# Kernel optimization log

Hardware: AMD Instinct MI355X
Metric: run time of the kernel (lower is better)

Reference implementation:

```python
import jax, jax.numpy as jnp
import numpy as np

B, S, D, H = 4, 2048, 1024, 16
DH = D // H
MAX_SEQ = 2048
OUT = 1024


def setup_inputs() -> dict:
    key = jax.random.key(0)
    ks = jax.random.split(key, 10)
    inp = {
        "x": jax.random.normal(ks[0], (B, S, D), dtype=jnp.float32),
        "src_key_padding_mask": jnp.ones((B, S), dtype=jnp.float32),  # 1 = valid token
        "pos_emb": jax.random.normal(ks[1], (1, MAX_SEQ, D), dtype=jnp.float32),
        "ln_gamma": jnp.ones((D,), dtype=jnp.float32),
        "ln_beta": jnp.zeros((D,), dtype=jnp.float32),
        "in_proj_weight": jax.random.normal(ks[2], (3 * D, D), dtype=jnp.float32) * (1.0 / np.sqrt(D)),
        "in_proj_bias": jnp.zeros((3 * D,), dtype=jnp.float32),
        "out_proj_weight": jax.random.normal(ks[3], (D, D), dtype=jnp.float32) * (1.0 / np.sqrt(D)),
        "out_proj_bias": jnp.zeros((D,), dtype=jnp.float32),
        "to_out_weight": jax.random.normal(ks[4], (OUT, D), dtype=jnp.float32) * (1.0 / np.sqrt(D)),
        "to_out_bias": jnp.zeros((OUT,), dtype=jnp.float32),
    }
    return inp


def _layernorm(x, gamma, beta, eps=1e-5):
    mu = jnp.mean(x, axis=-1, keepdims=True)
    var = jnp.mean(jnp.square(x - mu), axis=-1, keepdims=True)
    return (x - mu) * jax.lax.rsqrt(var + eps) * gamma + beta


def reference(x, src_key_padding_mask, pos_emb, ln_gamma, ln_beta,
              in_proj_weight, in_proj_bias, out_proj_weight, out_proj_bias,
              to_out_weight, to_out_bias):
    seq = x.shape[1]
    xn = _layernorm(x, ln_gamma, ln_beta)
    xp = xn + pos_emb[:, :seq, :]  # [B,S,D]

    # PyTorch quirk: 1.0 - mask.long() is a FLOAT tensor -> treated as ADDITIVE mask.
    add_mask = (1.0 - src_key_padding_mask)[:, None, None, :]  # [B,1,1,S]

    qkv = xp @ in_proj_weight.T + in_proj_bias  # [B,S,3D]
    q, k, v = jnp.split(qkv, 3, axis=-1)
    # [B,H,S,DH]
    q = q.reshape(B, seq, H, DH).transpose(0, 2, 1, 3)
    k = k.reshape(B, seq, H, DH).transpose(0, 2, 1, 3)
    v = v.reshape(B, seq, H, DH).transpose(0, 2, 1, 3)

    scores = jnp.einsum("bhqd,bhkd->bhqk", q, k) / jnp.sqrt(jnp.float32(DH))
    scores = scores + add_mask
    attn = jax.nn.softmax(scores, axis=-1)
    o = jnp.einsum("bhqk,bhkd->bhqd", attn, v)  # [B,H,S,DH]
    o = o.transpose(0, 2, 1, 3).reshape(B, seq, D)
    attn_out = o @ out_proj_weight.T + out_proj_bias

    return (xp + attn_out) @ to_out_weight.T + to_out_bias
```

## Files before the change

kernel.cpp:

```cpp
#include <hip/hip_runtime.h>
#include <stdint.h>
#include <stddef.h>

typedef unsigned short u16;
typedef __bf16 bf16x8 __attribute__((ext_vector_type(8)));
typedef float floatx4 __attribute__((ext_vector_type(4)));

#define B_  4
#define S_  2048
#define D_  1024
#define H_  16
#define DH_ 64

__device__ __forceinline__ float b2f(u16 u) {
  union { unsigned u; float f; } c; c.u = ((unsigned)u) << 16; return c.f;
}
__device__ __forceinline__ u16 f2b(float f) {
  union { float f; unsigned u; } c; c.f = f;
  unsigned u = c.u;
  u += 0x7fffu + ((u >> 16) & 1u);
  return (u16)(u >> 16);
}

__device__ __forceinline__ void gld_lds16(const u16* g, u16* l) {
  __builtin_amdgcn_global_load_lds(
      (const __attribute__((address_space(1))) unsigned int*)g,
      (__attribute__((address_space(3))) unsigned int*)l, 16, 0, 0);
}

__device__ __forceinline__ unsigned cvtpk(float lo, float hi) {
  unsigned r;
  asm("v_cvt_pk_bf16_f32 %0, %1, %2" : "=v"(r) : "v"(lo), "v"(hi));
  return r;
}

__device__ __forceinline__ float fexp2(float x) {
  float r; asm("v_exp_f32 %0, %1" : "=v"(r) : "v"(x)); return r;
}

#define PL32(a, b) asm("v_permlane32_swap_b32 %0, %1" : "+v"(a), "+v"(b))
#define PL16(a, b) asm("v_permlane16_swap_b32 %0, %1" : "+v"(a), "+v"(b))

union B8 { unsigned u[4]; bf16x8 v; };

__global__ __launch_bounds__(256) void cvt_f32_bf16(
    const float* __restrict__ src, u16* __restrict__ dst, int n)
{
  int i = (blockIdx.x * 256 + threadIdx.x) * 4;
  if (i >= n) return;
  float4 v = *(const float4*)(src + i);
  u16 o[4] __attribute__((aligned(8)));
  o[0] = f2b(v.x); o[1] = f2b(v.y); o[2] = f2b(v.z); o[3] = f2b(v.w);
  *(uint2*)(dst + i) = *(uint2*)o;
}

__global__ __launch_bounds__(256) void ln_pos_kernel(
    const float* __restrict__ x, const float* __restrict__ pos,
    const float* __restrict__ gamma, const float* __restrict__ beta,
    u16* __restrict__ xp)
{
  const int row = blockIdx.x;
  const int s = row & (S_ - 1);
  const int t = threadIdx.x;
  const int lane = t & 63, w = t >> 6;

  float4 xv = *(const float4*)(x + (size_t)row * D_ + t * 4);
  float f[4] = {xv.x, xv.y, xv.z, xv.w};
  float sum = f[0] + f[1] + f[2] + f[3];
  float sq  = f[0]*f[0] + f[1]*f[1] + f[2]*f[2] + f[3]*f[3];
#pragma unroll
  for (int m = 1; m < 64; m <<= 1) {
    sum += __shfl_xor(sum, m);
    sq  += __shfl_xor(sq, m);
  }
  __shared__ float red[8];
  if (lane == 0) { red[w] = sum; red[4 + w] = sq; }
  __syncthreads();
  sum = red[0] + red[1] + red[2] + red[3];
  sq  = red[4] + red[5] + red[6] + red[7];
  const float mu = sum * (1.f / D_);
  const float rstd = rsqrtf(fmaxf(sq * (1.f / D_) - mu * mu, 0.f) + 1e-5f);

  float4 gv = *(const float4*)(gamma + t * 4);
  float4 bv = *(const float4*)(beta + t * 4);
  float4 pv = *(const float4*)(pos + (size_t)s * D_ + t * 4);
  float g[4] = {gv.x, gv.y, gv.z, gv.w};
  float bb[4] = {bv.x, bv.y, bv.z, bv.w};
  float pp[4] = {pv.x, pv.y, pv.z, pv.w};
  u16 ov[4] __attribute__((aligned(8)));
#pragma unroll
  for (int i = 0; i < 4; ++i)
    ov[i] = f2b((f[i] - mu) * rstd * g[i] + bb[i] + pp[i]);
  *(uint2*)(xp + (size_t)row * D_ + t * 4) = *(uint2*)ov;
}

template<int HAS_BIAS, int HAS_RES, int OUT_F32>
__global__ __launch_bounds__(256) void gemm_bt(
    const u16* A, const u16* __restrict__ Bm,
    const float* __restrict__ bias, const u16* res,
    void* Cv, int M, int N, int K, int lda, int ldc)
{
  __shared__ u16 As[2][128 * 32];
  __shared__ u16 Bs[2][128 * 32];
  const int tid = threadIdx.x;
  const int lane = tid & 63, w = tid >> 6;
  const int quad = lane >> 4, l4 = lane & 15;
  const int wm = (w >> 1) * 64, wn = (w & 1) * 64;

  const int gx = gridDim.x;
  int lin = blockIdx.y * gx + blockIdx.x;
  lin = (lin & 7) * ((gx * gridDim.y) >> 3) + (lin >> 3);
  const int m0 = (lin / gx) * 128, n0 = (lin % gx) * 128;

  const u16* Ag = A + (size_t)m0 * lda;
  const u16* Bg = Bm + (size_t)n0 * K;

  const int s0 = tid, s1 = tid + 256;
  const int r0 = s0 >> 2, c0 = ((s0 & 3) - (r0 >> 1)) & 3;
  const int r1 = s1 >> 2, c1 = ((s1 & 3) - (r1 >> 1)) & 3;
  const int pA = (quad + (l4 >> 1)) & 3;

  floatx4 acc[4][4] = {};

  const int nk = K >> 5;
  gld_lds16(Ag + (size_t)r0 * lda + c0 * 8, &As[0][s0 * 8]);
  gld_lds16(Ag + (size_t)r1 * lda + c1 * 8, &As[0][s1 * 8]);
  gld_lds16(Bg + (size_t)r0 * K + c0 * 8, &Bs[0][s0 * 8]);
  gld_lds16(Bg + (size_t)r1 * K + c1 * 8, &Bs[0][s1 * 8]);
  __syncthreads();

  for (int kk = 0; kk < nk; ++kk) {
    const int cur = kk & 1;
    if (kk + 1 < nk) {
      const int k0 = (kk + 1) << 5;
      gld_lds16(Ag + (size_t)r0 * lda + k0 + c0 * 8, &As[cur ^ 1][s0 * 8]);
      gld_lds16(Ag + (size_t)r1 * lda + k0 + c1 * 8, &As[cur ^ 1][s1 * 8]);
      gld_lds16(Bg + (size_t)r0 * K + k0 + c0 * 8, &Bs[cur ^ 1][s0 * 8]);
      gld_lds16(Bg + (size_t)r1 * K + k0 + c1 * 8, &Bs[cur ^ 1][s1 * 8]);
    }
    bf16x8 af[4], bfr[4];
#pragma unroll
    for (int i = 0; i < 4; ++i)
      af[i] = *(const bf16x8*)&As[cur][(wm + i * 16 + l4) * 32 + pA * 8];
#pragma unroll
    for (int j = 0; j < 4; ++j)
      bfr[j] = *(const bf16x8*)&Bs[cur][(wn + j * 16 + l4) * 32 + pA * 8];
#pragma unroll
    for (int i = 0; i < 4; ++i)
#pragma unroll
      for (int j = 0; j < 4; ++j)
        acc[i][j] = __builtin_amdgcn_mfma_f32_16x16x32_bf16(af[i], bfr[j], acc[i][j], 0, 0, 0);
    __syncthreads();
  }

#pragma unroll
  for (int i = 0; i < 4; ++i) {
#pragma unroll
    for (int j = 0; j < 4; ++j) {
      const int col = n0 + wn + j * 16 + l4;
      float bvv = 0.f;
      if (HAS_BIAS) bvv = bias[col];
#pragma unroll
      for (int r = 0; r < 4; ++r) {
        const int row = m0 + wm + i * 16 + quad * 4 + r;
        float v = acc[i][j][r] + bvv;
        if (HAS_RES) v += b2f(res[(size_t)row * ldc + col]);
        v = fminf(fmaxf(v, -60000.f), 60000.f);
        if (OUT_F32) ((float*)Cv)[(size_t)row * ldc + col] = v;
        else         ((u16*)Cv)[(size_t)row * ldc + col] = f2b(v);
      }
    }
  }
}

__global__ __launch_bounds__(256, 3) void attn_kernel(
    u16* qkv, const float* __restrict__ mask)
{
  __shared__ u16 Ks[2][64 * 64];
  __shared__ u16 Vt[2][64 * 72];

  const int tid = threadIdx.x;
  const int lane = tid & 63, w = tid >> 6;
  const int quad = lane >> 4, l4 = lane & 15;
  const int qb = blockIdx.x;
  const int bh = blockIdx.y;
  const int b = bh >> 4, h = bh & 15;
  const int q0 = qb * 128;

  const size_t rstr = 3 * D_;
  u16* qbase = qkv + (size_t)b * S_ * rstr + h * DH_;

  bf16x8 qfrag[2][2];
#pragma unroll
  for (int qi = 0; qi < 2; ++qi) {
    const u16* qp = qbase + (size_t)(q0 + w * 32 + qi * 16 + l4) * rstr + quad * 8;
    qfrag[qi][0] = *(const bf16x8*)(qp);
    qfrag[qi][1] = *(const bf16x8*)(qp + 32);
  }

  const u16* kbase0 = qkv + (size_t)b * S_ * rstr + D_ + h * DH_;
  const u16* vbase0 = kbase0 + D_;
  const int vs = tid & 63, vd0 = (tid >> 6) * 16;

  B8 ones;
  ones.u[0] = ones.u[1] = ones.u[2] = ones.u[3] = 0x3f803f80u;

  floatx4 acc_o[2][4] = {};
  floatx4 acc_l[2] = {};
  u16 vreg[16] __attribute__((aligned(16)));

  {
#pragma unroll
    for (int t = 0; t < 2; ++t) {
      int sidx = tid + t * 256;
      int rr = sidx >> 3, ch = ((sidx & 7) - rr) & 7;
      gld_lds16(kbase0 + (size_t)rr * rstr + ch * 8, &Ks[0][sidx * 8]);
    }
    const u16* vp = vbase0 + (size_t)vs * rstr + vd0;
    *(uint4*)(vreg)     = *(const uint4*)(vp);
    *(uint4*)(vreg + 8) = *(const uint4*)(vp + 8);
  }
  __syncthreads();
#pragma unroll
  for (int d = 0; d < 16; ++d) Vt[0][(vd0 + d) * 72 + vs] = vreg[d];
  __syncthreads();

  int cur = 0;
  for (int j = 0; j < 32; ++j) {
    if (j < 31) {
      const u16* vp = vbase0 + ((size_t)(j + 1) * 64 + vs) * rstr + vd0;
      *(uint4*)(vreg)     = *(const uint4*)(vp);
      *(uint4*)(vreg + 8) = *(const uint4*)(vp + 8);
      const u16* kb = kbase0 + (size_t)(j + 1) * 64 * rstr;
#pragma unroll
      for (int t = 0; t < 2; ++t) {
        int sidx = tid + t * 256;
        int rr = sidx >> 3, ch = ((sidx & 7) - rr) & 7;
        gld_lds16(kb + (size_t)rr * rstr + ch * 8, &Ks[cur ^ 1][sidx * 8]);
      }
    }

    floatx4 accs[2][4] = {};
#pragma unroll
    for (int kc = 0; kc < 2; ++kc)
#pragma unroll
      for (int tj = 0; tj < 4; ++tj) {
        const int rk = tj * 16 + l4;
        bf16x8 kf = *(const bf16x8*)&Ks[cur][rk * 64 + (((kc * 4 + quad) + rk) & 7) * 8];
        accs[0][tj] = __builtin_amdgcn_mfma_f32_16x16x32_bf16(kf, qfrag[0][kc], accs[0][tj], 0, 0, 0);
        accs[1][tj] = __builtin_amdgcn_mfma_f32_16x16x32_bf16(kf, qfrag[1][kc], accs[1][tj], 0, 0, 0);
      }

    const float* mrow = mask + (size_t)b * S_ + j * 64 + quad * 4;
    float mterm[4][4];
#pragma unroll
    for (int tj = 0; tj < 4; ++tj) {
      float4 mv = *(const float4*)(mrow + tj * 16);
      mterm[tj][0] = fmaf(mv.x, -1.44269504f, 1.44269504f);
      mterm[tj][1] = fmaf(mv.y, -1.44269504f, 1.44269504f);
      mterm[tj][2] = fmaf(mv.z, -1.44269504f, 1.44269504f);
      mterm[tj][3] = fmaf(mv.w, -1.44269504f, 1.44269504f);
    }
    unsigned pk[2][4][2];
#pragma unroll
    for (int qi = 0; qi < 2; ++qi) {
#pragma unroll
      for (int tj = 0; tj < 4; ++tj) {
        float p0 = fexp2(fminf(fmaf(accs[qi][tj][0], 0.18033688f, mterm[tj][0]), 43.3f));
        float p1 = fexp2(fminf(fmaf(accs[qi][tj][1], 0.18033688f, mterm[tj][1]), 43.3f));
        float p2 = fexp2(fminf(fmaf(accs[qi][tj][2], 0.18033688f, mterm[tj][2]), 43.3f));
        float p3 = fexp2(fminf(fmaf(accs[qi][tj][3], 0.18033688f, mterm[tj][3]), 43.3f));
        pk[qi][tj][0] = cvtpk(p0, p1);
        pk[qi][tj][1] = cvtpk(p2, p3);
      }
    }

#pragma unroll
    for (int kc = 0; kc < 2; ++kc) {
      bf16x8 bfr[4];
#pragma unroll
      for (int tn = 0; tn < 4; ++tn)
        bfr[tn] = *(const bf16x8*)&Vt[cur][(tn * 16 + l4) * 72 + kc * 32 + quad * 8];
#pragma unroll
      for (int qi = 0; qi < 2; ++qi) {
        unsigned x0 = pk[qi][2 * kc][0], x1 = pk[qi][2 * kc + 1][0];
        unsigned y0 = pk[qi][2 * kc][1], y1 = pk[qi][2 * kc + 1][1];
        PL32(x0, x1); PL32(y0, y1);
        PL16(x0, x1); PL16(y0, y1);
        B8 pa; pa.u[0] = x0; pa.u[1] = y0; pa.u[2] = x1; pa.u[3] = y1;
        __builtin_amdgcn_s_setprio(1);
#pragma unroll
        for (int tn = 0; tn < 4; ++tn)
          acc_o[qi][tn] = __builtin_amdgcn_mfma_f32_16x16x32_bf16(pa.v, bfr[tn], acc_o[qi][tn], 0, 0, 0);
        acc_l[qi] = __builtin_amdgcn_mfma_f32_16x16x32_bf16(pa.v, ones.v, acc_l[qi], 0, 0, 0);
        __builtin_amdgcn_s_setprio(0);
      }
    }

    if (j < 31) {
#pragma unroll
      for (int d = 0; d < 16; ++d) Vt[cur ^ 1][(vd0 + d) * 72 + vs] = vreg[d];
    }

    __syncthreads();
    cur ^= 1;
  }

#pragma unroll
  for (int qi = 0; qi < 2; ++qi) {
    float inv[4];
#pragma unroll
    for (int r = 0; r < 4; ++r) inv[r] = 1.0f / acc_l[qi][r];
#pragma unroll
    for (int tn = 0; tn < 4; ++tn) {
#pragma unroll
      for (int r = 0; r < 4; ++r) {
        const int row = q0 + w * 32 + qi * 16 + quad * 4 + r;
        const int col = h * DH_ + tn * 16 + l4;
        qkv[((size_t)b * S_ + row) * rstr + col] = f2b(acc_o[qi][tn][r] * inv[r]);
      }
    }
  }
}

extern "C" void kernel_launch(void* const* d_in, const int* in_sizes, int n_in,
                              void* d_out, int out_size, void* d_ws, size_t ws_size,
                              hipStream_t stream) {
  const float* x    = (const float*)d_in[0];
  const float* mask = (const float*)d_in[1];
  const float* pos  = (const float*)d_in[2];
  const float* gam  = (const float*)d_in[3];
  const float* bet  = (const float*)d_in[4];
  const float* wqkv = (const float*)d_in[5];
  const float* bqkv = (const float*)d_in[6];
  const float* wo   = (const float*)d_in[7];
  const float* bo   = (const float*)d_in[8];
  const float* wt   = (const float*)d_in[9];
  const float* bt   = (const float*)d_in[10];
  float* out = (float*)d_out;

  char* ws = (char*)d_ws;
  u16* qkvb = (u16*)(ws);
  u16* xp   = (u16*)(ws + (size_t)50331648);

  u16* wqkv_b = (u16*)d_out;
  u16* wo_b   = (u16*)((char*)d_out + (size_t)6291456);
  u16* wt_b   = qkvb;

  const int nqkv = 3 * D_ * D_;
  const int nd   = D_ * D_;

  cvt_f32_bf16<<<nqkv / 1024, 256, 0, stream>>>(wqkv, wqkv_b, nqkv);
  cvt_f32_bf16<<<nd   / 1024, 256, 0, stream>>>(wo,   wo_b,   nd);
  ln_pos_kernel<<<B_ * S_, 256, 0, stream>>>(x, pos, gam, bet, xp);
  gemm_bt<1, 0, 0><<<dim3(3 * D_ / 128, B_ * S_ / 128), 256, 0, stream>>>(
      xp, wqkv_b, bqkv, nullptr, qkvb, B_ * S_, 3 * D_, D_, D_, 3 * D_);
  attn_kernel<<<dim3(S_ / 128, B_ * H_), 256, 0, stream>>>(qkvb, mask);
  gemm_bt<1, 1, 0><<<dim3(D_ / 128, B_ * S_ / 128), 256, 0, stream>>>(
      qkvb, wo_b, bo, xp, xp, B_ * S_, D_, D_, 3 * D_, D_);
  cvt_f32_bf16<<<nd / 1024, 256, 0, stream>>>(wt, wt_b, nd);
  gemm_bt<1, 0, 1><<<dim3(D_ / 128, B_ * S_ / 128), 256, 0, stream>>>(
      xp, wt_b, bt, nullptr, out, B_ * S_, D_, D_, D_, D_);
}
```

Before: 384.0 us.

## Add 256x256-tile triple-buffered GEMM for the QKV projection

```diff
diff --git a/kernel.cpp b/kernel.cpp
--- a/kernel.cpp
+++ b/kernel.cpp
@@ -163,6 +163,97 @@
 #pragma unroll
       for (int r = 0; r < 4; ++r) {
         const int row = m0 + wm + i * 16 + quad * 4 + r;
+        float v = acc[i][j][r] + bvv;
+        if (HAS_RES) v += b2f(res[(size_t)row * ldc + col]);
+        v = fminf(fmaxf(v, -60000.f), 60000.f);
+        if (OUT_F32) ((float*)Cv)[(size_t)row * ldc + col] = v;
+        else         ((u16*)Cv)[(size_t)row * ldc + col] = f2b(v);
+      }
+    }
+  }
+}
+
+template<int HAS_BIAS, int HAS_RES, int OUT_F32>
+__global__ __launch_bounds__(512, 2) void gemm_bt256(
+    const u16* A, const u16* __restrict__ Bm,
+    const float* __restrict__ bias, const u16* res,
+    void* Cv, int M, int N, int K, int lda, int ldc)
+{
+  __shared__ u16 As[3][256 * 32];
+  __shared__ u16 Bs[3][256 * 32];
+  const int tid = threadIdx.x;
+  const int lane = tid & 63, w = tid >> 6;
+  const int quad = lane >> 4, l4 = lane & 15;
+  const int wr = (w >> 2) * 128, wc = (w & 3) * 64;
+
+  const int gx = gridDim.x;
+  int lin = blockIdx.y * gx + blockIdx.x;
+  lin = (lin & 7) * ((gx * gridDim.y) >> 3) + (lin >> 3);
+  const int m0 = (lin / gx) * 256, n0 = (lin % gx) * 256;
+
+  const u16* Ag = A + (size_t)m0 * lda;
+  const u16* Bg = Bm + (size_t)n0 * K;
+
+  const int s0 = tid, s1 = tid + 512;
+  const int r0 = s0 >> 2, c0 = ((s0 & 3) - (r0 >> 1)) & 3;
+  const int r1 = s1 >> 2, c1 = ((s1 & 3) - (r1 >> 1)) & 3;
+  const int pA = (quad + (l4 >> 1)) & 3;
+
+  floatx4 acc[8][4] = {};
+
+  const int nk = K >> 5;
+
+#define STG256(kt, buf)                                                      \
+  {                                                                          \
+    const int k0 = (kt) << 5;                                                \
+    gld_lds16(Ag + (size_t)r0 * lda + k0 + c0 * 8, &As[buf][s0 * 8]);        \
+    gld_lds16(Ag + (size_t)r1 * lda + k0 + c1 * 8, &As[buf][s1 * 8]);        \
+    gld_lds16(Bg + (size_t)r0 * K + k0 + c0 * 8, &Bs[buf][s0 * 8]);          \
+    gld_lds16(Bg + (size_t)r1 * K + k0 + c1 * 8, &Bs[buf][s1 * 8]);          \
+  }
+
+  STG256(0, 0);
+  STG256(1, 1);
+
+  for (int kk = 0; kk < nk; ++kk) {
+    const int cur = kk % 3;
+    if (kk + 2 < nk) { asm volatile("s_waitcnt vmcnt(4)" ::: "memory"); }
+    else             { asm volatile("s_waitcnt vmcnt(0)" ::: "memory"); }
+    asm volatile("s_barrier" ::: "memory");
+    if (kk + 2 < nk) STG256(kk + 2, (kk + 2) % 3);
+
+    bf16x8 bfr[4];
+#pragma unroll
+    for (int n = 0; n < 4; ++n)
+      bfr[n] = *(const bf16x8*)&Bs[cur][(wc + n * 16 + l4) * 32 + pA * 8];
+#pragma unroll
+    for (int mh = 0; mh < 2; ++mh) {
+      bf16x8 af[4];
+#pragma unroll
+      for (int mm = 0; mm < 4; ++mm)
+        af[mm] = *(const bf16x8*)&As[cur][(wr + mh * 64 + mm * 16 + l4) * 32 + pA * 8];
+      __builtin_amdgcn_s_setprio(1);
+#pragma unroll
+      for (int mm = 0; mm < 4; ++mm)
+#pragma unroll
+        for (int n = 0; n < 4; ++n)
+          acc[mh * 4 + mm][n] = __builtin_amdgcn_mfma_f32_16x16x32_bf16(
+              af[mm], bfr[n], acc[mh * 4 + mm][n], 0, 0, 0);
+      __builtin_amdgcn_s_setprio(0);
+    }
+  }
+#undef STG256
+
+#pragma unroll
+  for (int i = 0; i < 8; ++i) {
+#pragma unroll
+    for (int j = 0; j < 4; ++j) {
+      const int col = n0 + wc + j * 16 + l4;
+      float bvv = 0.f;
+      if (HAS_BIAS) bvv = bias[col];
+#pragma unroll
+      for (int r = 0; r < 4; ++r) {
+        const int row = m0 + wr + i * 16 + quad * 4 + r;
         float v = acc[i][j][r] + bvv;
         if (HAS_RES) v += b2f(res[(size_t)row * ldc + col]);
         v = fminf(fmaxf(v, -60000.f), 60000.f);
@@ -353,7 +444,7 @@
   cvt_f32_bf16<<<nqkv / 1024, 256, 0, stream>>>(wqkv, wqkv_b, nqkv);
   cvt_f32_bf16<<<nd   / 1024, 256, 0, stream>>>(wo,   wo_b,   nd);
   ln_pos_kernel<<<B_ * S_, 256, 0, stream>>>(x, pos, gam, bet, xp);
-  gemm_bt<1, 0, 0><<<dim3(3 * D_ / 128, B_ * S_ / 128), 256, 0, stream>>>(
+  gemm_bt256<1, 0, 0><<<dim3(3 * D_ / 256, B_ * S_ / 256), 512, 0, stream>>>(
       xp, wqkv_b, bqkv, nullptr, qkvb, B_ * S_, 3 * D_, D_, D_, 3 * D_);
   attn_kernel<<<dim3(S_ / 128, B_ * H_), 256, 0, stream>>>(qkvb, mask);
   gemm_bt<1, 1, 0><<<dim3(D_ / 128, B_ * S_ / 128), 256, 0, stream>>>(
```

Result: slower. 402.4 us (+4.8%).
